# Optimization experiments

Measured on AMD Instinct MI355X. Metric: run time of the kernel, lower is better.

The kernel has to match this reference:

```python
import jax, jax.numpy as jnp
import numpy as np

N_ENT = 50000
N_USR = 10000
N_NODES = N_ENT + N_USR
D = 64            # entity_dim
AE_H = [128, 32]  # autoencoder hidden dims
CONV = [32, 16]   # graph conv output dims
R = 16            # n_relations
E = 1920000       # n_edges (avg degree 32)
B = 4096          # scoring batch


def setup_inputs() -> dict:
    key = jax.random.key(0)
    ks = jax.random.split(key, 24)
    s = 0.05
    rn = lambda k, shp: jax.random.normal(k, shp, jnp.float32) * s
    inp = {
        # int graph / batch inputs
        "users": jax.random.randint(ks[0], (B,), 0, N_USR),
        "items": jax.random.randint(ks[1], (B,), 0, N_ENT),
        "edge_src": jax.random.randint(ks[2], (E,), 0, N_NODES),
        "edge_dst": jax.random.randint(ks[3], (E,), 0, N_NODES),
        "edge_rel": jax.random.randint(ks[4], (E,), 0, R),
        # embeddings
        "entity_emb": rn(ks[5], (N_ENT, D)),
        "user_emb": rn(ks[6], (N_USR, D)),
        # autoencoder (weights stored [in, out])
        "enc_W0": rn(ks[7], (D, AE_H[0])), "enc_b0": jnp.zeros((AE_H[0],), jnp.float32),
        "enc_W1": rn(ks[8], (AE_H[0], AE_H[1])), "enc_b1": jnp.zeros((AE_H[1],), jnp.float32),
        "dec_W0": rn(ks[9], (AE_H[1], AE_H[0])), "dec_b0": jnp.zeros((AE_H[0],), jnp.float32),
        "dec_W1": rn(ks[10], (AE_H[0], D)), "dec_b1": jnp.zeros((D,), jnp.float32),
        # conv layer 1: input_dim=32 -> W_r [R, 64, 32], linear [64 -> 32]
        "Wr1": rn(ks[11], (R, 2 * CONV[0], CONV[0])),
        "lin_W1": rn(ks[12], (2 * CONV[0], CONV[0])), "lin_b1": jnp.zeros((CONV[0],), jnp.float32),
        # conv layer 2: input_dim=32 -> W_r [R, 64, 32], linear [64 -> 16]
        "Wr2": rn(ks[13], (R, 2 * CONV[0], CONV[0])),
        "lin_W2": rn(ks[14], (2 * CONV[0], CONV[1])), "lin_b2": jnp.zeros((CONV[1],), jnp.float32),
    }
    return inp


def _graph_conv(x, edge_src, edge_dst, edge_rel, W_r, lin_W, lin_b):
    # gate logit = sum_j (concat(h_dst, h_src) @ W_r[rel])_j
    #            = concat(h_dst, h_src) . W_r[rel].sum(-1)  (exact identity)
    w_sum = W_r.sum(axis=-1)                      # [R, 2*in]
    h_dst = x[edge_dst]                            # [E, in]
    h_src = x[edge_src]                            # [E, in]
    c = jnp.concatenate([h_dst, h_src], axis=-1)   # [E, 2*in]
    gate = jax.nn.sigmoid(jnp.sum(c * w_sum[edge_rel], axis=-1, keepdims=True))  # [E,1]
    weighted = h_src * gate                        # [E, in]
    n = x.shape[0]
    agg_sum = jax.ops.segment_sum(weighted, edge_dst, num_segments=n)           # [N, in]
    cnt = jax.ops.segment_sum(jnp.ones((edge_dst.shape[0], 1), x.dtype), edge_dst, num_segments=n)
    agg = jnp.where(cnt > 0, agg_sum / jnp.maximum(cnt, 1.0), 0.0)              # scatter-mean
    combined = jnp.concatenate([x, agg], axis=-1)  # [N, 2*in]
    return jax.nn.leaky_relu(combined @ lin_W + lin_b, negative_slope=0.01)


def reference(entity_emb, user_emb,
              enc_W0, enc_b0, enc_W1, enc_b1,
              dec_W0, dec_b0, dec_W1, dec_b1,
              Wr1, lin_W1, lin_b1, Wr2, lin_W2, lin_b2,
              users, items, edge_src, edge_dst, edge_rel):
    all_emb = jnp.concatenate([entity_emb, user_emb], axis=0)  # [N, 64]
    # autoencoder: ReLU between layers, none at the end of encode/decode
    encoded = jax.nn.relu(all_emb @ enc_W0 + enc_b0) @ enc_W1 + enc_b1  # [N, 32]
    decoded = jax.nn.relu(encoded @ dec_W0 + dec_b0) @ dec_W1 + dec_b1  # [N, 64]
    ae_loss = jnp.mean((decoded - all_emb) ** 2)

    x1 = _graph_conv(encoded, edge_src, edge_dst, edge_rel, Wr1, lin_W1, lin_b1)  # [N, 32]
    x2 = _graph_conv(x1, edge_src, edge_dst, edge_rel, Wr2, lin_W2, lin_b2)       # [N, 16]
    final = jnp.concatenate([x1, x2], axis=-1)  # [N, 48]

    user_nodes = N_ENT + users
    scores = jnp.sum(final[user_nodes] * final[items], axis=-1)  # [B]
    return scores, ae_loss
```

## Files before the change

kernel.cpp:

```cpp
#include <hip/hip_runtime.h>
#include <hip/hip_fp16.h>
#include <math.h>

#define N_ENT 50000
#define N_USR 10000
#define NN    60000
#define DD    64
#define H0    128
#define ENCD  32
#define RR    16
#define NB    256
#define BSH   8
#define NBU   235

__device__ __forceinline__ float4 ld4(const float* p){ return *reinterpret_cast<const float4*>(p); }
__device__ __forceinline__ void st4(float* p, float4 v){ *reinterpret_cast<float4*>(p) = v; }

__global__ __launch_bounds__(256) void k_wsum(const float* __restrict__ Wr1, const float* __restrict__ Wr2,
                                              float* __restrict__ wsum){
  int i = blockIdx.x*256 + threadIdx.x;
  if (i >= 2*RR*DD) return;
  const float* Wr = (i < RR*DD) ? Wr1 : Wr2;
  int loc = i & (RR*DD - 1);
  const float* p = Wr + (size_t)loc*32;
  float s = 0.f;
  #pragma unroll
  for (int k=0;k<32;k++) s += p[k];
  wsum[i] = s;
}

__global__ __launch_bounds__(256) void k_enc1(const float* __restrict__ ent, const float* __restrict__ usr,
    const float* __restrict__ W0, const float* __restrict__ b0, float* __restrict__ h1t){
  int n = blockIdx.x*256 + threadIdx.x;
  if (n >= NN) return;
  int j0 = blockIdx.y * 16;
  const float* xr = (n < N_ENT) ? (ent + (size_t)n*DD) : (usr + (size_t)(n-N_ENT)*DD);
  float xv[DD];
  #pragma unroll
  for (int q=0;q<DD/4;q++){ float4 v = ld4(xr + 4*q); xv[4*q]=v.x; xv[4*q+1]=v.y; xv[4*q+2]=v.z; xv[4*q+3]=v.w; }
  float acc[16];
  #pragma unroll
  for (int t=0;t<16;t++) acc[t] = b0[j0+t];
  const float* w = W0 + j0;
  #pragma unroll
  for (int d=0; d<DD; d++){
    #pragma unroll
    for (int t=0;t<16;t++) acc[t] = fmaf(xv[d], w[(size_t)d*H0 + t], acc[t]);
  }
  float* out = h1t + ((size_t)blockIdx.y * NN + n) * 16;
  #pragma unroll
  for (int q=0;q<4;q++){
    float4 v; v.x=fmaxf(acc[4*q],0.f); v.y=fmaxf(acc[4*q+1],0.f); v.z=fmaxf(acc[4*q+2],0.f); v.w=fmaxf(acc[4*q+3],0.f);
    st4(out + 4*q, v);
  }
}

__global__ __launch_bounds__(256) void k_enc2(const float* __restrict__ h1t, const float* __restrict__ W1,
    const float* __restrict__ b1, float* __restrict__ enc){
  int n = blockIdx.x*256 + threadIdx.x;
  if (n >= NN) return;
  float acc[32];
  #pragma unroll
  for (int t=0;t<32;t++) acc[t] = b1[t];
  for (int tj=0; tj<8; tj++){
    const float* hr = h1t + ((size_t)tj * NN + n) * 16;
    float h[16];
    #pragma unroll
    for (int q=0;q<4;q++){ float4 v = ld4(hr+4*q); h[4*q]=v.x; h[4*q+1]=v.y; h[4*q+2]=v.z; h[4*q+3]=v.w; }
    const float* w = W1 + (size_t)tj*16*ENCD;
    #pragma unroll
    for (int jj=0;jj<16;jj++){
      #pragma unroll
      for (int t=0;t<32;t++) acc[t] = fmaf(h[jj], w[(size_t)jj*ENCD + t], acc[t]);
    }
  }
  float* out = enc + (size_t)n*ENCD;
  #pragma unroll
  for (int q=0;q<8;q++){ float4 v; v.x=acc[4*q]; v.y=acc[4*q+1]; v.z=acc[4*q+2]; v.w=acc[4*q+3]; st4(out+4*q, v); }
}

__global__ __launch_bounds__(256) void k_dec1(const float* __restrict__ enc, const float* __restrict__ dW0,
    const float* __restrict__ db0, float* __restrict__ h2t){
  int n = blockIdx.x*256 + threadIdx.x;
  if (n >= NN) return;
  int j0 = blockIdx.y * 16;
  const float* xr = enc + (size_t)n*ENCD;
  float xv[ENCD];
  #pragma unroll
  for (int q=0;q<ENCD/4;q++){ float4 v = ld4(xr + 4*q); xv[4*q]=v.x; xv[4*q+1]=v.y; xv[4*q+2]=v.z; xv[4*q+3]=v.w; }
  float acc[16];
  #pragma unroll
  for (int t=0;t<16;t++) acc[t] = db0[j0+t];
  const float* w = dW0 + j0;
  #pragma unroll
  for (int d=0; d<ENCD; d++){
    #pragma unroll
    for (int t=0;t<16;t++) acc[t] = fmaf(xv[d], w[(size_t)d*H0 + t], acc[t]);
  }
  float* out = h2t + ((size_t)blockIdx.y * NN + n) * 16;
  #pragma unroll
  for (int q=0;q<4;q++){
    float4 v; v.x=fmaxf(acc[4*q],0.f); v.y=fmaxf(acc[4*q+1],0.f); v.z=fmaxf(acc[4*q+2],0.f); v.w=fmaxf(acc[4*q+3],0.f);
    st4(out + 4*q, v);
  }
}

__global__ __launch_bounds__(256) void k_dec2(const float* __restrict__ h2t, const float* __restrict__ dW1,
    const float* __restrict__ db1, const float* __restrict__ ent, const float* __restrict__ usr,
    float* __restrict__ loss_out){
  int n = blockIdx.x*256 + threadIdx.x;
  int k0 = blockIdx.y * 32;
  float part = 0.f;
  if (n < NN){
    float acc[32];
    #pragma unroll
    for (int t=0;t<32;t++) acc[t] = db1[k0+t];
    for (int tj=0; tj<8; tj++){
      const float* hr = h2t + ((size_t)tj * NN + n) * 16;
      float h[16];
      #pragma unroll
      for (int q=0;q<4;q++){ float4 v = ld4(hr+4*q); h[4*q]=v.x; h[4*q+1]=v.y; h[4*q+2]=v.z; h[4*q+3]=v.w; }
      const float* w = dW1 + (size_t)tj*16*DD + k0;
      #pragma unroll
      for (int jj=0;jj<16;jj++){
        #pragma unroll
        for (int t=0;t<32;t++) acc[t] = fmaf(h[jj], w[(size_t)jj*DD + t], acc[t]);
      }
    }
    const float* xr = (n < N_ENT) ? (ent + (size_t)n*DD + k0) : (usr + (size_t)(n-N_ENT)*DD + k0);
    #pragma unroll
    for (int t=0;t<32;t++){ float d_ = acc[t] - xr[t]; part = fmaf(d_, d_, part); }
  }
  #pragma unroll
  for (int off=32; off>0; off>>=1) part += __shfl_down(part, off, 64);
  __shared__ float sred[4];
  if ((threadIdx.x & 63)==0) sred[threadIdx.x>>6] = part;
  __syncthreads();
  if (threadIdx.x==0){
    float s = (sred[0]+sred[1]+sred[2]+sred[3]) * (1.0f/((float)NN*(float)DD));
    atomicAdd(loss_out, s);
  }
}

__global__ __launch_bounds__(256) void k_hist256(const int* __restrict__ edst, int* __restrict__ bktCnt, int E_){
  __shared__ int h[NB];
  h[threadIdx.x]=0;
  __syncthreads();
  int i0 = blockIdx.x*4096;
  #pragma unroll
  for (int k=0;k<16;k++){
    int e = i0 + k*256 + threadIdx.x;
    if (e < E_) atomicAdd(&h[((unsigned)edst[e])>>BSH], 1);
  }
  __syncthreads();
  int c = h[threadIdx.x];
  if (c) atomicAdd(&bktCnt[threadIdx.x], c);
}

__global__ __launch_bounds__(256) void k_scan256(const int* __restrict__ bktCnt, int* __restrict__ bktBase){
  __shared__ int wps[4];
  int t = threadIdx.x;
  int v = bktCnt[t];
  int x = v;
  #pragma unroll
  for (int off=1; off<64; off<<=1){
    int y = __shfl_up(x, off, 64);
    if ((t & 63) >= off) x += y;
  }
  if ((t & 63) == 63) wps[t >> 6] = x;
  __syncthreads();
  if (t < 4){
    int wv = wps[t];
    int wx = wv;
    #pragma unroll
    for (int off=1; off<4; off<<=1){
      int y = __shfl_up(wx, off, 4);
      if (t >= off) wx += y;
    }
    wps[t] = wx - wv;
  }
  __syncthreads();
  bktBase[t] = (x - v) + wps[t >> 6];
}

__global__ __launch_bounds__(256) void k_bucketA(const int* __restrict__ esrc, const int* __restrict__ edst,
    const int* __restrict__ erel, const int* __restrict__ bktBase, int* __restrict__ bktFill,
    unsigned* __restrict__ bktData, int E_){
  __shared__ int h[NB];
  __shared__ int gbase[NB];
  h[threadIdx.x]=0;
  __syncthreads();
  int i0 = blockIdx.x*4096;
  int dcache[16];
  #pragma unroll
  for (int k=0;k<16;k++){
    int e = i0 + k*256 + threadIdx.x;
    int d = (e < E_) ? edst[e] : -1;
    dcache[k] = d;
    if (d >= 0) atomicAdd(&h[((unsigned)d)>>BSH], 1);
  }
  __syncthreads();
  {
    int c = h[threadIdx.x];
    int off = c ? atomicAdd(&bktFill[threadIdx.x], c) : 0;
    gbase[threadIdx.x] = bktBase[threadIdx.x] + off;
    h[threadIdx.x] = 0;
  }
  __syncthreads();
  #pragma unroll
  for (int k=0;k<16;k++){
    int e = i0 + k*256 + threadIdx.x;
    if (e >= E_) continue;
    int d = dcache[k];
    int b = ((unsigned)d) >> BSH;
    int slot = atomicAdd(&h[b], 1);
    unsigned rec = (unsigned)esrc[e] | ((unsigned)erel[e] << 16) | ((unsigned)(d & 0xFF) << 20);
    bktData[(size_t)gbase[b] + slot] = rec;
  }
}

__global__ __launch_bounds__(256) void k_buildB(const unsigned* __restrict__ bktData,
    const int* __restrict__ bktBase, const int* __restrict__ bktCnt,
    int* __restrict__ rowp, int* __restrict__ packed){
  __shared__ int cnt[NB];
  __shared__ int start[NB];
  __shared__ int wps[4];
  int b = blockIdx.x;
  int base = bktBase[b];
  int n = bktCnt[b];
  int t = threadIdx.x;
  cnt[t] = 0;
  __syncthreads();
  for (int i=t; i<n; i+=256) atomicAdd(&cnt[(bktData[base+i] >> 20) & 0xFF], 1);
  __syncthreads();
  int v = cnt[t];
  cnt[t] = 0;
  int x = v;
  #pragma unroll
  for (int off=1; off<64; off<<=1){
    int y = __shfl_up(x, off, 64);
    if ((t & 63) >= off) x += y;
  }
  if ((t & 63) == 63) wps[t >> 6] = x;
  __syncthreads();
  if (t < 4){
    int wv = wps[t];
    int wx = wv;
    #pragma unroll
    for (int off=1; off<4; off<<=1){
      int y = __shfl_up(wx, off, 4);
      if (t >= off) wx += y;
    }
    wps[t] = wx - wv;
  }
  __syncthreads();
  int sv = (x - v) + wps[t >> 6];
  start[t] = sv;
  int node = (b << BSH) + t;
  if (node <= NN) rowp[node] = base + sv;
  __syncthreads();
  for (int i=t; i<n; i+=256){
    unsigned r = bktData[base+i];
    int dl = (r >> 20) & 0xFF;
    int p = start[dl] + atomicAdd(&cnt[dl], 1);
    packed[base + p] = (int)r;
  }
}

__global__ __launch_bounds__(256) void k_dots(const float* __restrict__ x, const float* __restrict__ wsum,
    float* __restrict__ dA, __half* __restrict__ dbrec, __half* __restrict__ xrec){
  __shared__ float wl[RR*DD];
  for (int i = threadIdx.x; i < RR*DD; i += 256){
    int r = i & 15; int j = i >> 4;
    wl[i] = wsum[r*DD + j];
  }
  __syncthreads();
  int t = blockIdx.x*256 + threadIdx.x;
  if (t >= NN*RR) return;
  int n = t >> 4, r = t & 15;
  const float* xr = x + (size_t)n*ENCD;
  float a = 0.f, b = 0.f;
  float xlo = 0.f, xhi = 0.f;
  #pragma unroll
  for (int q=0;q<8;q++){
    float4 v = ld4(xr + 4*q);
    int j = 4*q;
    if (r >= j && r < j+4){ float tmp[4]={v.x,v.y,v.z,v.w}; xlo = tmp[r-j]; }
    if (r+16 >= j && r+16 < j+4){ float tmp[4]={v.x,v.y,v.z,v.w}; xhi = tmp[r+16-j]; }
    a = fmaf(v.x, wl[(j+0)*16 + r], a);
    a = fmaf(v.y, wl[(j+1)*16 + r], a);
    a = fmaf(v.z, wl[(j+2)*16 + r], a);
    a = fmaf(v.w, wl[(j+3)*16 + r], a);
    b = fmaf(v.x, wl[(32+j+0)*16 + r], b);
    b = fmaf(v.y, wl[(32+j+1)*16 + r], b);
    b = fmaf(v.z, wl[(32+j+2)*16 + r], b);
    b = fmaf(v.w, wl[(32+j+3)*16 + r], b);
  }
  dA[t] = a;
  dbrec[t] = __float2half(b);
  xrec[(size_t)n*32 + r]      = __float2half(xlo);
  xrec[(size_t)n*32 + 16 + r] = __float2half(xhi);
}

__global__ __launch_bounds__(256) void k_gates(const int* __restrict__ packed,
    const int* __restrict__ bktBase, const int* __restrict__ bktCnt,
    const float* __restrict__ dA, const __half* __restrict__ dbrec, __half* __restrict__ gat){
  int b = blockIdx.x >> 2, g = blockIdx.x & 3;
  int base = bktBase[b], n = bktCnt[b];
  int lo = (n*g) >> 2, hi = (n*(g+1)) >> 2;
  for (int i = lo + (int)threadIdx.x; i < hi; i += 256){
    int p = packed[base+i];
    int s = p & 0xFFFF;
    int r = (p >> 16) & 15;
    int dl = (p >> 20) & 0xFF;
    int dst = (b << BSH) | dl;
    float z = dA[dst*16 + r] + __half2float(dbrec[s*16 + r]);
    gat[base+i] = __float2half(1.f/(1.f + __expf(-z)));
  }
}

__global__ __launch_bounds__(256) void k_agg(const __half2* __restrict__ xrec2, const int* __restrict__ packed,
    const __half* __restrict__ gat, const int* __restrict__ rowp, float* __restrict__ agg){
  int node = blockIdx.x*16 + (threadIdx.x >> 4);
  int l = threadIdx.x & 15;
  if (node >= NN) return;
  int beg = rowp[node], end = rowp[node+1];
  float ax = 0.f, ay = 0.f;
  #pragma unroll 4
  for (int i = beg; i < end; i++){
    int p = packed[i];
    int s = p & 0xFFFF;
    float g = __half2float(gat[i]);
    float2 fx = __half22float2(xrec2[(size_t)s*16 + l]);
    ax = fmaf(fx.x, g, ax);
    ay = fmaf(fx.y, g, ay);
  }
  int deg = end - beg;
  float inv = (deg > 0) ? 1.f/(float)deg : 0.f;
  float2 o; o.x = ax*inv; o.y = ay*inv;
  *reinterpret_cast<float2*>(&agg[(size_t)node*ENCD + 2*l]) = o;
}

__global__ __launch_bounds__(256) void k_lin(const float* __restrict__ x, const float* __restrict__ agg,
    const float* __restrict__ W, const float* __restrict__ b, float* __restrict__ out, int outd){
  int n = blockIdx.x*256 + threadIdx.x;
  if (n >= NN) return;
  int k0 = blockIdx.y * 16;
  const float* xr = x   + (size_t)n*ENCD;
  const float* ar = agg + (size_t)n*ENCD;
  float xv[32], av[32];
  #pragma unroll
  for (int q=0;q<8;q++){ float4 v = ld4(xr+4*q); xv[4*q]=v.x; xv[4*q+1]=v.y; xv[4*q+2]=v.z; xv[4*q+3]=v.w; }
  #pragma unroll
  for (int q=0;q<8;q++){ float4 v = ld4(ar+4*q); av[4*q]=v.x; av[4*q+1]=v.y; av[4*q+2]=v.z; av[4*q+3]=v.w; }
  float acc[16];
  #pragma unroll
  for (int t=0;t<16;t++) acc[t] = b[k0+t];
  #pragma unroll
  for (int j=0;j<32;j++){
    #pragma unroll
    for (int t=0;t<16;t++) acc[t] = fmaf(xv[j], W[(size_t)j*outd + k0 + t], acc[t]);
  }
  #pragma unroll
  for (int j=0;j<32;j++){
    #pragma unroll
    for (int t=0;t<16;t++) acc[t] = fmaf(av[j], W[(size_t)(32+j)*outd + k0 + t], acc[t]);
  }
  float* o = out + (size_t)n*outd + k0;
  #pragma unroll
  for (int q=0;q<4;q++){
    float4 v;
    float a0=acc[4*q],a1=acc[4*q+1],a2=acc[4*q+2],a3=acc[4*q+3];
    v.x = a0>0.f? a0 : 0.01f*a0;
    v.y = a1>0.f? a1 : 0.01f*a1;
    v.z = a2>0.f? a2 : 0.01f*a2;
    v.w = a3>0.f? a3 : 0.01f*a3;
    st4(o + 4*q, v);
  }
}

__global__ __launch_bounds__(256) void k_score(const float* __restrict__ x1, const float* __restrict__ x2,
    const int* __restrict__ users, const int* __restrict__ items, float* __restrict__ out, int Bn){
  int b = blockIdx.x*256 + threadIdx.x;
  if (b >= Bn) return;
  int u  = N_ENT + users[b];
  int it = items[b];
  const float* a1 = x1 + (size_t)u*32;
  const float* c1 = x1 + (size_t)it*32;
  const float* a2 = x2 + (size_t)u*16;
  const float* c2 = x2 + (size_t)it*16;
  float s = 0.f;
  #pragma unroll
  for (int q=0;q<8;q++){
    float4 va=ld4(a1+4*q), vb=ld4(c1+4*q);
    s = fmaf(va.x,vb.x,s); s = fmaf(va.y,vb.y,s); s = fmaf(va.z,vb.z,s); s = fmaf(va.w,vb.w,s);
  }
  #pragma unroll
  for (int q=0;q<4;q++){
    float4 va=ld4(a2+4*q), vb=ld4(c2+4*q);
    s = fmaf(va.x,vb.x,s); s = fmaf(va.y,vb.y,s); s = fmaf(va.z,vb.z,s); s = fmaf(va.w,vb.w,s);
  }
  out[b] = s;
}

extern "C" void kernel_launch(void* const* d_in, const int* in_sizes, int n_in,
                              void* d_out, int out_size, void* d_ws, size_t ws_size,
                              hipStream_t stream){
  const int*   users   = (const int*)d_in[0];
  const int*   items   = (const int*)d_in[1];
  const int*   esrc    = (const int*)d_in[2];
  const int*   edst    = (const int*)d_in[3];
  const int*   erel    = (const int*)d_in[4];
  const float* ent     = (const float*)d_in[5];
  const float* usr     = (const float*)d_in[6];
  const float* enc_W0  = (const float*)d_in[7];
  const float* enc_b0  = (const float*)d_in[8];
  const float* enc_W1  = (const float*)d_in[9];
  const float* enc_b1  = (const float*)d_in[10];
  const float* dec_W0  = (const float*)d_in[11];
  const float* dec_b0  = (const float*)d_in[12];
  const float* dec_W1  = (const float*)d_in[13];
  const float* dec_b1  = (const float*)d_in[14];
  const float* Wr1     = (const float*)d_in[15];
  const float* lin_W1  = (const float*)d_in[16];
  const float* lin_b1  = (const float*)d_in[17];
  const float* Wr2     = (const float*)d_in[18];
  const float* lin_W2  = (const float*)d_in[19];
  const float* lin_b2  = (const float*)d_in[20];
  const int E = in_sizes[2];
  const int B = in_sizes[0];

  char* wp = (char*)d_ws;
  auto carve = [&](size_t bytes)->char*{ char* p = wp; wp += (bytes + 255) & ~(size_t)255; return p; };
  float* enc    = (float*)carve((size_t)NN*32*4);
  float* x1     = (float*)carve((size_t)NN*32*4);
  float* x2     = (float*)carve((size_t)NN*16*4);
  float* agg    = (float*)carve((size_t)NN*32*4);
  float* h1t    = (float*)carve((size_t)NN*128*4);
  float* wsum   = (float*)carve((size_t)2*RR*DD*4);
  float* dA     = (float*)carve((size_t)NN*RR*4);
  __half* dbrec = (__half*)carve((size_t)NN*RR*2);
  __half* xrec  = (__half*)carve((size_t)NN*32*2);
  __half* gat   = (__half*)carve((size_t)E*2);
  int*   packed = (int*)  carve((size_t)E*4);
  int*   bktCnt = (int*)  carve((size_t)2*NB*4);
  int*   bktFill= bktCnt + NB;
  int*   bktBase= (int*)  carve(NB*4);
  int*   rowp   = (int*)  carve(((size_t)NN+1)*4);
  unsigned* bktData = (unsigned*)h1t;

  const int nbN = (NN + 255)/256;
  const int nbT = (E + 4095)/4096;
  const int nbD = (NN*RR + 255)/256;
  dim3 blk(256);

  hipMemsetAsync(d_out, 0, (size_t)out_size*sizeof(float), stream);
  hipMemsetAsync(bktCnt, 0, (size_t)2*NB*sizeof(int), stream);

  k_wsum <<<dim3((2*RR*DD+255)/256), blk, 0, stream>>>(Wr1, Wr2, wsum);
  k_enc1 <<<dim3(nbN, 8), blk, 0, stream>>>(ent, usr, enc_W0, enc_b0, h1t);
  k_enc2 <<<dim3(nbN), blk, 0, stream>>>(h1t, enc_W1, enc_b1, enc);
  k_dec1 <<<dim3(nbN, 8), blk, 0, stream>>>(enc, dec_W0, dec_b0, h1t);
  k_dec2 <<<dim3(nbN, 2), blk, 0, stream>>>(h1t, dec_W1, dec_b1, ent, usr, ((float*)d_out) + B);

  k_hist256<<<nbT, blk, 0, stream>>>(edst, bktCnt, E);
  k_scan256<<<1, blk, 0, stream>>>(bktCnt, bktBase);
  k_bucketA<<<nbT, blk, 0, stream>>>(esrc, edst, erel, bktBase, bktFill, bktData, E);
  k_buildB <<<NBU, blk, 0, stream>>>(bktData, bktBase, bktCnt, rowp, packed);

  k_dots <<<nbD, blk, 0, stream>>>(enc, wsum, dA, dbrec, xrec);
  k_gates<<<NBU*4, blk, 0, stream>>>(packed, bktBase, bktCnt, dA, dbrec, gat);
  k_agg  <<<(NN+15)/16, blk, 0, stream>>>((const __half2*)xrec, packed, gat, rowp, agg);
  k_lin  <<<dim3(nbN, 2), blk, 0, stream>>>(enc, agg, lin_W1, lin_b1, x1, 32);

  k_dots <<<nbD, blk, 0, stream>>>(x1, wsum + RR*DD, dA, dbrec, xrec);
  k_gates<<<NBU*4, blk, 0, stream>>>(packed, bktBase, bktCnt, dA, dbrec, gat);
  k_agg  <<<(NN+15)/16, blk, 0, stream>>>((const __half2*)xrec, packed, gat, rowp, agg);
  k_lin  <<<dim3(nbN, 1), blk, 0, stream>>>(x1, agg, lin_W2, lin_b2, x2, 16);

  k_score<<<(B+255)/256, blk, 0, stream>>>(x1, x2, users, items, (float*)d_out, B);
}
```

Baseline: 443.3 us.

## Fuse autoencoder encode/decode layers into one LDS-staged kernel

Replaces the four separate autoencoder kernels with a single kernel that handles 64 nodes per block. Inputs, hidden activations and encodings are staged in shared memory, and each wave computes a slice of the output features. This removes the 128-wide hidden activation round trips through global memory and three kernel launches. The cost is lower parallelism (938 blocks) and higher shared-memory use per block, which may reduce occupancy. Because the hidden buffer is gone, bktData now gets its own workspace allocation.

```diff
diff --git a/kernel.cpp b/kernel.cpp
--- a/kernel.cpp
+++ b/kernel.cpp
@@ -29,117 +29,126 @@
   wsum[i] = s;
 }
 
-__global__ __launch_bounds__(256) void k_enc1(const float* __restrict__ ent, const float* __restrict__ usr,
-    const float* __restrict__ W0, const float* __restrict__ b0, float* __restrict__ h1t){
-  int n = blockIdx.x*256 + threadIdx.x;
-  if (n >= NN) return;
-  int j0 = blockIdx.y * 16;
-  const float* xr = (n < N_ENT) ? (ent + (size_t)n*DD) : (usr + (size_t)(n-N_ENT)*DD);
-  float xv[DD];
-  #pragma unroll
-  for (int q=0;q<DD/4;q++){ float4 v = ld4(xr + 4*q); xv[4*q]=v.x; xv[4*q+1]=v.y; xv[4*q+2]=v.z; xv[4*q+3]=v.w; }
-  float acc[16];
-  #pragma unroll
-  for (int t=0;t<16;t++) acc[t] = b0[j0+t];
-  const float* w = W0 + j0;
-  #pragma unroll
-  for (int d=0; d<DD; d++){
-    #pragma unroll
-    for (int t=0;t<16;t++) acc[t] = fmaf(xv[d], w[(size_t)d*H0 + t], acc[t]);
-  }
-  float* out = h1t + ((size_t)blockIdx.y * NN + n) * 16;
-  #pragma unroll
-  for (int q=0;q<4;q++){
-    float4 v; v.x=fmaxf(acc[4*q],0.f); v.y=fmaxf(acc[4*q+1],0.f); v.z=fmaxf(acc[4*q+2],0.f); v.w=fmaxf(acc[4*q+3],0.f);
-    st4(out + 4*q, v);
-  }
-}
-
-__global__ __launch_bounds__(256) void k_enc2(const float* __restrict__ h1t, const float* __restrict__ W1,
-    const float* __restrict__ b1, float* __restrict__ enc){
-  int n = blockIdx.x*256 + threadIdx.x;
-  if (n >= NN) return;
-  float acc[32];
-  #pragma unroll
-  for (int t=0;t<32;t++) acc[t] = b1[t];
-  for (int tj=0; tj<8; tj++){
-    const float* hr = h1t + ((size_t)tj * NN + n) * 16;
-    float h[16];
-    #pragma unroll
-    for (int q=0;q<4;q++){ float4 v = ld4(hr+4*q); h[4*q]=v.x; h[4*q+1]=v.y; h[4*q+2]=v.z; h[4*q+3]=v.w; }
-    const float* w = W1 + (size_t)tj*16*ENCD;
-    #pragma unroll
-    for (int jj=0;jj<16;jj++){
-      #pragma unroll
-      for (int t=0;t<32;t++) acc[t] = fmaf(h[jj], w[(size_t)jj*ENCD + t], acc[t]);
-    }
-  }
-  float* out = enc + (size_t)n*ENCD;
-  #pragma unroll
-  for (int q=0;q<8;q++){ float4 v; v.x=acc[4*q]; v.y=acc[4*q+1]; v.z=acc[4*q+2]; v.w=acc[4*q+3]; st4(out+4*q, v); }
-}
-
-__global__ __launch_bounds__(256) void k_dec1(const float* __restrict__ enc, const float* __restrict__ dW0,
-    const float* __restrict__ db0, float* __restrict__ h2t){
-  int n = blockIdx.x*256 + threadIdx.x;
-  if (n >= NN) return;
-  int j0 = blockIdx.y * 16;
-  const float* xr = enc + (size_t)n*ENCD;
-  float xv[ENCD];
-  #pragma unroll
-  for (int q=0;q<ENCD/4;q++){ float4 v = ld4(xr + 4*q); xv[4*q]=v.x; xv[4*q+1]=v.y; xv[4*q+2]=v.z; xv[4*q+3]=v.w; }
-  float acc[16];
-  #pragma unroll
-  for (int t=0;t<16;t++) acc[t] = db0[j0+t];
-  const float* w = dW0 + j0;
-  #pragma unroll
-  for (int d=0; d<ENCD; d++){
-    #pragma unroll
-    for (int t=0;t<16;t++) acc[t] = fmaf(xv[d], w[(size_t)d*H0 + t], acc[t]);
-  }
-  float* out = h2t + ((size_t)blockIdx.y * NN + n) * 16;
-  #pragma unroll
-  for (int q=0;q<4;q++){
-    float4 v; v.x=fmaxf(acc[4*q],0.f); v.y=fmaxf(acc[4*q+1],0.f); v.z=fmaxf(acc[4*q+2],0.f); v.w=fmaxf(acc[4*q+3],0.f);
-    st4(out + 4*q, v);
-  }
-}
-
-__global__ __launch_bounds__(256) void k_dec2(const float* __restrict__ h2t, const float* __restrict__ dW1,
-    const float* __restrict__ db1, const float* __restrict__ ent, const float* __restrict__ usr,
-    float* __restrict__ loss_out){
-  int n = blockIdx.x*256 + threadIdx.x;
-  int k0 = blockIdx.y * 32;
+__global__ __launch_bounds__(256) void k_ae(const float* __restrict__ ent, const float* __restrict__ usr,
+    const float* __restrict__ eW0, const float* __restrict__ eb0,
+    const float* __restrict__ eW1, const float* __restrict__ eb1,
+    const float* __restrict__ dW0c, const float* __restrict__ db0,
+    const float* __restrict__ dW1c, const float* __restrict__ db1,
+    float* __restrict__ enc, float* __restrict__ loss_out){
+  __shared__ float xs[DD][65];
+  __shared__ float hs[H0][65];
+  __shared__ float es[ENCD][65];
+  __shared__ float sred[4];
+  int t = threadIdx.x;
+  int nl = t & 63;
+  int wid = __builtin_amdgcn_readfirstlane(t >> 6);
+
+  {
+    int n2 = t >> 2;
+    int d0 = (t & 3) * 16;
+    int gnode = blockIdx.x*64 + n2;
+    if (gnode < NN){
+      const float* xr = (gnode < N_ENT) ? ent + (size_t)gnode*DD : usr + (size_t)(gnode-N_ENT)*DD;
+      #pragma unroll
+      for (int q=0;q<4;q++){
+        float4 v = ld4(xr + d0 + 4*q);
+        xs[d0+4*q+0][n2]=v.x; xs[d0+4*q+1][n2]=v.y; xs[d0+4*q+2][n2]=v.z; xs[d0+4*q+3][n2]=v.w;
+      }
+    } else {
+      #pragma unroll
+      for (int q=0;q<16;q++) xs[d0+q][n2]=0.f;
+    }
+  }
+  __syncthreads();
+
+  {
+    int j0 = wid*32;
+    float acc[32];
+    #pragma unroll
+    for (int k=0;k<32;k++) acc[k]=eb0[j0+k];
+    #pragma unroll 4
+    for (int d=0;d<DD;d++){
+      float x = xs[d][nl];
+      const float* w = eW0 + (size_t)d*H0 + j0;
+      #pragma unroll
+      for (int k=0;k<32;k++) acc[k]=fmaf(x,w[k],acc[k]);
+    }
+    #pragma unroll
+    for (int k=0;k<32;k++) hs[j0+k][nl]=fmaxf(acc[k],0.f);
+  }
+  __syncthreads();
+
+  {
+    int k0 = wid*8;
+    float acc[8];
+    #pragma unroll
+    for (int k=0;k<8;k++) acc[k]=eb1[k0+k];
+    #pragma unroll 4
+    for (int j=0;j<H0;j++){
+      float hv = hs[j][nl];
+      const float* w = eW1 + (size_t)j*ENCD + k0;
+      #pragma unroll
+      for (int k=0;k<8;k++) acc[k]=fmaf(hv,w[k],acc[k]);
+    }
+    #pragma unroll
+    for (int k=0;k<8;k++) es[k0+k][nl]=acc[k];
+  }
+  __syncthreads();
+
+  {
+    int n2 = t >> 2;
+    int k2 = (t & 3) * 8;
+    int gnode = blockIdx.x*64 + n2;
+    if (gnode < NN){
+      float4 a, b;
+      a.x=es[k2+0][n2]; a.y=es[k2+1][n2]; a.z=es[k2+2][n2]; a.w=es[k2+3][n2];
+      b.x=es[k2+4][n2]; b.y=es[k2+5][n2]; b.z=es[k2+6][n2]; b.w=es[k2+7][n2];
+      st4(enc + (size_t)gnode*ENCD + k2, a);
+      st4(enc + (size_t)gnode*ENCD + k2 + 4, b);
+    }
+  }
+
+  {
+    int j0 = wid*32;
+    float acc[32];
+    #pragma unroll
+    for (int k=0;k<32;k++) acc[k]=db0[j0+k];
+    #pragma unroll 4
+    for (int d=0;d<ENCD;d++){
+      float x = es[d][nl];
+      const float* w = dW0c + (size_t)d*H0 + j0;
+      #pragma unroll
+      for (int k=0;k<32;k++) acc[k]=fmaf(x,w[k],acc[k]);
+    }
+    #pragma unroll
+    for (int k=0;k<32;k++) hs[j0+k][nl]=fmaxf(acc[k],0.f);
+  }
+  __syncthreads();
+
   float part = 0.f;
-  if (n < NN){
-    float acc[32];
-    #pragma unroll
-    for (int t=0;t<32;t++) acc[t] = db1[k0+t];
-    for (int tj=0; tj<8; tj++){
-      const float* hr = h2t + ((size_t)tj * NN + n) * 16;
-      float h[16];
-      #pragma unroll
-      for (int q=0;q<4;q++){ float4 v = ld4(hr+4*q); h[4*q]=v.x; h[4*q+1]=v.y; h[4*q+2]=v.z; h[4*q+3]=v.w; }
-      const float* w = dW1 + (size_t)tj*16*DD + k0;
-      #pragma unroll
-      for (int jj=0;jj<16;jj++){
-        #pragma unroll
-        for (int t=0;t<32;t++) acc[t] = fmaf(h[jj], w[(size_t)jj*DD + t], acc[t]);
-      }
-    }
-    const float* xr = (n < N_ENT) ? (ent + (size_t)n*DD + k0) : (usr + (size_t)(n-N_ENT)*DD + k0);
-    #pragma unroll
-    for (int t=0;t<32;t++){ float d_ = acc[t] - xr[t]; part = fmaf(d_, d_, part); }
+  {
+    int c0 = wid*16;
+    float acc[16];
+    #pragma unroll
+    for (int k=0;k<16;k++) acc[k]=db1[c0+k];
+    #pragma unroll 4
+    for (int j=0;j<H0;j++){
+      float hv = hs[j][nl];
+      const float* w = dW1c + (size_t)j*DD + c0;
+      #pragma unroll
+      for (int k=0;k<16;k++) acc[k]=fmaf(hv,w[k],acc[k]);
+    }
+    int gnode = blockIdx.x*64 + nl;
+    if (gnode < NN){
+      #pragma unroll
+      for (int k=0;k<16;k++){ float d_ = acc[k]-xs[c0+k][nl]; part = fmaf(d_,d_,part); }
+    }
   }
   #pragma unroll
   for (int off=32; off>0; off>>=1) part += __shfl_down(part, off, 64);
-  __shared__ float sred[4];
-  if ((threadIdx.x & 63)==0) sred[threadIdx.x>>6] = part;
-  __syncthreads();
-  if (threadIdx.x==0){
-    float s = (sred[0]+sred[1]+sred[2]+sred[3]) * (1.0f/((float)NN*(float)DD));
-    atomicAdd(loss_out, s);
-  }
+  if ((t&63)==0) sred[t>>6] = part;
+  __syncthreads();
+  if (t==0) atomicAdd(loss_out, (sred[0]+sred[1]+sred[2]+sred[3]) * (1.0f/((float)NN*(float)DD)));
 }
 
 __global__ __launch_bounds__(256) void k_hist256(const int* __restrict__ edst, int* __restrict__ bktCnt, int E_){
@@ -436,18 +445,17 @@
   float* x1     = (float*)carve((size_t)NN*32*4);
   float* x2     = (float*)carve((size_t)NN*16*4);
   float* agg    = (float*)carve((size_t)NN*32*4);
-  float* h1t    = (float*)carve((size_t)NN*128*4);
   float* wsum   = (float*)carve((size_t)2*RR*DD*4);
   float* dA     = (float*)carve((size_t)NN*RR*4);
   __half* dbrec = (__half*)carve((size_t)NN*RR*2);
   __half* xrec  = (__half*)carve((size_t)NN*32*2);
   __half* gat   = (__half*)carve((size_t)E*2);
   int*   packed = (int*)  carve((size_t)E*4);
+  unsigned* bktData = (unsigned*)carve((size_t)E*4);
   int*   bktCnt = (int*)  carve((size_t)2*NB*4);
   int*   bktFill= bktCnt + NB;
   int*   bktBase= (int*)  carve(NB*4);
   int*   rowp   = (int*)  carve(((size_t)NN+1)*4);
-  unsigned* bktData = (unsigned*)h1t;
 
   const int nbN = (NN + 255)/256;
   const int nbT = (E + 4095)/4096;
@@ -458,10 +466,9 @@
   hipMemsetAsync(bktCnt, 0, (size_t)2*NB*sizeof(int), stream);
 
   k_wsum <<<dim3((2*RR*DD+255)/256), blk, 0, stream>>>(Wr1, Wr2, wsum);
-  k_enc1 <<<dim3(nbN, 8), blk, 0, stream>>>(ent, usr, enc_W0, enc_b0, h1t);
-  k_enc2 <<<dim3(nbN), blk, 0, stream>>>(h1t, enc_W1, enc_b1, enc);
-  k_dec1 <<<dim3(nbN, 8), blk, 0, stream>>>(enc, dec_W0, dec_b0, h1t);
-  k_dec2 <<<dim3(nbN, 2), blk, 0, stream>>>(h1t, dec_W1, dec_b1, ent, usr, ((float*)d_out) + B);
+  k_ae   <<<dim3((NN+63)/64), blk, 0, stream>>>(ent, usr, enc_W0, enc_b0, enc_W1, enc_b1,
+                                                dec_W0, dec_b0, dec_W1, dec_b1,
+                                                enc, ((float*)d_out) + B);
 
   k_hist256<<<nbT, blk, 0, stream>>>(edst, bktCnt, E);
   k_scan256<<<1, blk, 0, stream>>>(bktCnt, bktBase);
```

Result: faster. 393.5 us (-11.2%).
